# Performance work log

Measured on AMD Instinct MI355X. Metric: run time of the kernel, lower is better.

## Reference

```python
import jax, jax.numpy as jnp
import numpy as np

B, K, VDIM, QDIM, NHID, SE_INNER = 8192, 6, 2048, 1024, 1024, 128

def setup_inputs() -> dict:
    key = jax.random.key(0)
    ks = jax.random.split(key, 10)
    w = lambda k, shape: jax.random.normal(k, shape, dtype=jnp.float32) * 0.02
    return {
        "v": jax.random.normal(ks[0], (B, K, VDIM), dtype=jnp.float32),
        "q": jax.random.normal(ks[1], (B, QDIM), dtype=jnp.float32),
        "mask": (jax.random.uniform(ks[2], (B, K)) > 0.5).astype(jnp.float32),
        "W1": w(ks[3], (NHID, VDIM + QDIM)),   # FCNet weight-normed Linear (effective weight)
        "b1": jnp.zeros((NHID,), jnp.float32),
        "Wl": w(ks[4], (1, NHID)),             # logits Linear(num_hid, 1)
        "bl": jnp.zeros((1,), jnp.float32),
        "Wse1": w(ks[5], (SE_INNER, 1)),       # SELayer fc1, no bias
        "Wse2": w(ks[6], (1, SE_INNER)),       # SELayer fc2, no bias
        "Wf": w(ks[7], (VDIM, 1)),             # final_att_proj Linear(1, v_dim)
        "bf": jnp.zeros((VDIM,), jnp.float32),
    }

def reference(v, q, mask, W1, b1, Wl, bl, Wse1, Wse2, Wf, bf):
    Bn, Kn, _ = v.shape
    # logits(v, q): concat q to every object, FCNet (Linear+ReLU), Linear->1 (dropout is identity at eval)
    qe = jnp.broadcast_to(q[:, None, :], (Bn, Kn, q.shape[-1]))
    vq = jnp.concatenate([v, qe], axis=-1)                       # [B,K,vd+qd]
    joint = jax.nn.relu(jnp.einsum('bkf,hf->bkh', vq, W1) + b1)  # [B,K,NHID]
    logits = jnp.einsum('bkh,oh->bko', joint, Wl) + bl           # [B,K,1]
    single_att = jax.nn.softmax(logits, axis=1)
    w = logits                                                   # view(mask_b, 6, -1) is identity here
    w_ctx = w * mask[..., None]                                  # [B,K,1]
    # per-role sum over the 5 complementary roles == total - self (exact complement index sets)
    neigh = jnp.sum(w_ctx, axis=1, keepdims=True) - w_ctx        # [B,K,1]
    x = neigh[..., None]                                         # [B,K,1,1]
    # SE gate: FC(1->128) -> ReLU -> FC(128->1) -> Sigmoid; out = x * (1 - y)
    y = jax.nn.sigmoid(jax.nn.relu(x @ Wse1.T) @ Wse2.T)          # [B,K,1,1]
    gated = x * (1.0 - y)
    # final_att_proj(gated + w[:,role].unsqueeze(-1)) : Linear(1 -> v_dim)
    upd = (gated + w[..., None]) @ Wf.T + bf                     # [B,K,1,VDIM]
    context_erased_att = upd.reshape(Bn * Kn, 1, upd.shape[-1])  # [B*K,1,VDIM]
    return single_att, context_erased_att
```

## Files before the change

kernel.cpp:

```cpp
#include <hip/hip_runtime.h>

#define B_SZ   8192
#define KOBJ   6
#define VD     2048
#define QD     1024
#define NHID_  1024
#define SEIN   128
#define M_TOT  (B_SZ * KOBJ)
#define K_TOT  (VD + QD)

typedef __bf16 bf16x8 __attribute__((ext_vector_type(8)));
typedef float  f32x4  __attribute__((ext_vector_type(4)));
typedef unsigned int uint4v __attribute__((ext_vector_type(4)));

__device__ __forceinline__ unsigned short f2bf(float f) {
    unsigned u = __builtin_bit_cast(unsigned, f);
    u += 0x7fffu + ((u >> 16) & 1u);
    return (unsigned short)(u >> 16);
}

__global__ __launch_bounds__(256) void conv_w1(const float* __restrict__ W1,
                                               unsigned short* __restrict__ W1b,
                                               int n4) {
    int i = blockIdx.x * 256 + threadIdx.x;
    if (i < n4) {
        float4 f = ((const float4*)W1)[i];
        unsigned lo = (unsigned)f2bf(f.x) | ((unsigned)f2bf(f.y) << 16);
        unsigned hi = (unsigned)f2bf(f.z) | ((unsigned)f2bf(f.w) << 16);
        ((uint2*)W1b)[i] = make_uint2(lo, hi);
    }
}

#define LDA 40
__global__ __launch_bounds__(256) void gemm_logits(
    const float* __restrict__ v, const float* __restrict__ q,
    const unsigned short* __restrict__ W1b,
    const float* __restrict__ b1, const float* __restrict__ Wl,
    float* __restrict__ logits)
{
    __shared__ unsigned short At[128 * LDA];
    __shared__ unsigned short Bt[128 * LDA];

    const int tid  = threadIdx.x;
    const int bid  = blockIdx.x;
    const int nb   = bid & 7;
    const int mb   = bid >> 3;
    const int m0   = mb * 128;
    const int n0   = nb * 128;
    const int wave = tid >> 6, lane = tid & 63;
    const int quad = lane >> 4, l16 = lane & 15;
    const int wr   = (wave >> 1) * 64, wc = (wave & 1) * 64;

    f32x4 acc[4][4] = {};

    for (int kk = 0; kk < K_TOT; kk += 32) {
        __syncthreads();
        const bool isq = (kk >= VD);
        #pragma unroll
        for (int it = 0; it < 4; ++it) {
            int s   = tid + it * 256;
            int row = s >> 3, c4 = s & 7;
            int m   = m0 + row;
            const float* src = isq ? (q + (size_t)(m / KOBJ) * QD + (kk - VD) + c4 * 4)
                                   : (v + (size_t)m * VD + kk + c4 * 4);
            float4 f = *(const float4*)src;
            unsigned lo = (unsigned)f2bf(f.x) | ((unsigned)f2bf(f.y) << 16);
            unsigned hi = (unsigned)f2bf(f.z) | ((unsigned)f2bf(f.w) << 16);
            *(uint2*)&At[row * LDA + c4 * 4] = make_uint2(lo, hi);
        }
        #pragma unroll
        for (int it = 0; it < 2; ++it) {
            int s  = tid + it * 256;
            int n  = s >> 2, kg = s & 3;
            uint4v d = *(const uint4v*)(W1b + (size_t)(n0 + n) * K_TOT + kk + kg * 8);
            *(uint4v*)&Bt[n * LDA + kg * 8] = d;
        }
        __syncthreads();
        bf16x8 af[4], bfr[4];
        #pragma unroll
        for (int i = 0; i < 4; ++i)
            af[i] = __builtin_bit_cast(bf16x8, *(const uint4v*)&At[(wr + i * 16 + l16) * LDA + quad * 8]);
        #pragma unroll
        for (int j = 0; j < 4; ++j)
            bfr[j] = __builtin_bit_cast(bf16x8, *(const uint4v*)&Bt[(wc + j * 16 + l16) * LDA + quad * 8]);
        #pragma unroll
        for (int i = 0; i < 4; ++i)
            #pragma unroll
            for (int j = 0; j < 4; ++j)
                acc[i][j] = __builtin_amdgcn_mfma_f32_16x16x32_bf16(af[i], bfr[j], acc[i][j], 0, 0, 0);
    }

    #pragma unroll
    for (int i = 0; i < 4; ++i) {
        #pragma unroll
        for (int r = 0; r < 4; ++r) {
            int m = m0 + wr + i * 16 + quad * 4 + r;
            float sum = 0.f;
            #pragma unroll
            for (int j = 0; j < 4; ++j) {
                int n = n0 + wc + j * 16 + l16;
                float h = fmaxf(acc[i][j][r] + b1[n], 0.f);
                sum = fmaf(h, Wl[n], sum);
            }
            sum += __shfl_xor(sum, 1);
            sum += __shfl_xor(sum, 2);
            sum += __shfl_xor(sum, 4);
            sum += __shfl_xor(sum, 8);
            if (l16 == 0) atomicAdd(&logits[m], sum);
        }
    }
}

__global__ __launch_bounds__(256) void se_kernel(
    const float* __restrict__ logits, const float* __restrict__ mask,
    const float* __restrict__ bl,
    const float* __restrict__ Wse1, const float* __restrict__ Wse2,
    float* __restrict__ out_att, float* __restrict__ s_buf)
{
    int b = blockIdx.x * 256 + threadIdx.x;
    if (b >= B_SZ) return;
    float w[KOBJ];
    float blv = bl[0];
    #pragma unroll
    for (int k = 0; k < KOBJ; ++k) w[k] = logits[b * KOBJ + k] + blv;

    float mx = w[0];
    #pragma unroll
    for (int k = 1; k < KOBJ; ++k) mx = fmaxf(mx, w[k]);
    float e[KOBJ], den = 0.f;
    #pragma unroll
    for (int k = 0; k < KOBJ; ++k) { e[k] = __expf(w[k] - mx); den += e[k]; }
    float rden = 1.f / den;
    #pragma unroll
    for (int k = 0; k < KOBJ; ++k) out_att[b * KOBJ + k] = e[k] * rden;

    float wc[KOBJ], tot = 0.f;
    #pragma unroll
    for (int k = 0; k < KOBJ; ++k) { wc[k] = w[k] * mask[b * KOBJ + k]; tot += wc[k]; }

    #pragma unroll
    for (int k = 0; k < KOBJ; ++k) {
        float x = tot - wc[k];
        float a = 0.f;
        for (int i = 0; i < SEIN; ++i)
            a = fmaf(fmaxf(x * Wse1[i], 0.f), Wse2[i], a);
        float y = 1.f / (1.f + __expf(-a));
        s_buf[b * KOBJ + k] = x * (1.f - y) + w[k];
    }
}

__global__ __launch_bounds__(256) void out_writer(
    const float* __restrict__ s_buf, const float* __restrict__ Wf,
    const float* __restrict__ bfv, float* __restrict__ out)
{
    int m = blockIdx.x;
    float s = s_buf[m];
    const float4* wf4 = (const float4*)Wf;
    const float4* bf4 = (const float4*)bfv;
    float4* o4 = (float4*)(out + (size_t)m * VD);
    #pragma unroll
    for (int it = 0; it < VD / 4 / 256; ++it) {
        int t = threadIdx.x + it * 256;
        float4 wv = wf4[t], bv = bf4[t];
        float4 r;
        r.x = fmaf(s, wv.x, bv.x);
        r.y = fmaf(s, wv.y, bv.y);
        r.z = fmaf(s, wv.z, bv.z);
        r.w = fmaf(s, wv.w, bv.w);
        o4[t] = r;
    }
}

extern "C" void kernel_launch(void* const* d_in, const int* in_sizes, int n_in,
                              void* d_out, int out_size, void* d_ws, size_t ws_size,
                              hipStream_t stream) {
    const float* v    = (const float*)d_in[0];
    const float* q    = (const float*)d_in[1];
    const float* mask = (const float*)d_in[2];
    const float* W1   = (const float*)d_in[3];
    const float* b1   = (const float*)d_in[4];
    const float* Wl   = (const float*)d_in[5];
    const float* bl   = (const float*)d_in[6];
    const float* Wse1 = (const float*)d_in[7];
    const float* Wse2 = (const float*)d_in[8];
    const float* Wf   = (const float*)d_in[9];
    const float* bfv  = (const float*)d_in[10];
    float* out = (float*)d_out;

    char* ws = (char*)d_ws;
    unsigned short* W1b = (unsigned short*)ws;
    float* logits = (float*)(ws + 6291456);
    float* s_buf  = (float*)(ws + 6291456 + 196608);

    hipMemsetAsync(logits, 0, M_TOT * sizeof(float), stream);
    conv_w1<<<(NHID_ * K_TOT / 4 + 255) / 256, 256, 0, stream>>>(W1, W1b, NHID_ * K_TOT / 4);
    gemm_logits<<<(M_TOT / 128) * (NHID_ / 128), 256, 0, stream>>>(v, q, W1b, b1, Wl, logits);
    se_kernel<<<(B_SZ + 255) / 256, 256, 0, stream>>>(logits, mask, bl, Wse1, Wse2, out, s_buf);
    out_writer<<<M_TOT, 256, 0, stream>>>(s_buf, Wf, bfv, out + M_TOT);
}
```

Baseline: 1.200 ms.

## Pre-convert activations to bf16 and stream GEMM tiles via direct global-to-LDS loads

Adds separate passes that convert v and q to bf16, using the output buffer as scratch, before the GEMM runs. The GEMM then loads bf16 tiles straight into LDS with global_load_lds and reads them with an XOR swizzle instead of padded rows. This is meant to remove per-tile fp32 loads, conversions and register round trips from the GEMM loop, and to halve the bytes each of the eight N-blocks reads for the A operand. In exchange it adds a full extra read and write of v (about 400MB fp32 in, 200MB bf16 out) plus three kernel launches.

```diff
diff --git a/kernel.cpp b/kernel.cpp
--- a/kernel.cpp
+++ b/kernel.cpp
@@ -19,27 +19,30 @@
     return (unsigned short)(u >> 16);
 }
 
-__global__ __launch_bounds__(256) void conv_w1(const float* __restrict__ W1,
-                                               unsigned short* __restrict__ W1b,
-                                               int n4) {
+__global__ __launch_bounds__(256) void conv_bf16(const float* __restrict__ src,
+                                                 unsigned short* __restrict__ dst,
+                                                 int n8) {
     int i = blockIdx.x * 256 + threadIdx.x;
-    if (i < n4) {
-        float4 f = ((const float4*)W1)[i];
-        unsigned lo = (unsigned)f2bf(f.x) | ((unsigned)f2bf(f.y) << 16);
-        unsigned hi = (unsigned)f2bf(f.z) | ((unsigned)f2bf(f.w) << 16);
-        ((uint2*)W1b)[i] = make_uint2(lo, hi);
-    }
-}
-
-#define LDA 40
+    if (i < n8) {
+        float4 f0 = ((const float4*)src)[2 * i];
+        float4 f1 = ((const float4*)src)[2 * i + 1];
+        uint4v d;
+        d[0] = (unsigned)f2bf(f0.x) | ((unsigned)f2bf(f0.y) << 16);
+        d[1] = (unsigned)f2bf(f0.z) | ((unsigned)f2bf(f0.w) << 16);
+        d[2] = (unsigned)f2bf(f1.x) | ((unsigned)f2bf(f1.y) << 16);
+        d[3] = (unsigned)f2bf(f1.z) | ((unsigned)f2bf(f1.w) << 16);
+        ((uint4v*)dst)[i] = d;
+    }
+}
+
 __global__ __launch_bounds__(256) void gemm_logits(
-    const float* __restrict__ v, const float* __restrict__ q,
+    const unsigned short* __restrict__ vb, const unsigned short* __restrict__ qb,
     const unsigned short* __restrict__ W1b,
     const float* __restrict__ b1, const float* __restrict__ Wl,
     float* __restrict__ logits)
 {
-    __shared__ unsigned short At[128 * LDA];
-    __shared__ unsigned short Bt[128 * LDA];
+    __shared__ unsigned short At[128 * 32];
+    __shared__ unsigned short Bt[128 * 32];
 
     const int tid  = threadIdx.x;
     const int bid  = blockIdx.x;
@@ -51,38 +54,56 @@
     const int quad = lane >> 4, l16 = lane & 15;
     const int wr   = (wave >> 1) * 64, wc = (wave & 1) * 64;
 
+    int rowA[2], chA[2];
+    const unsigned short* gav[2];
+    const unsigned short* gaq[2];
+    const unsigned short* gb[2];
+    unsigned short* ldsA[2];
+    unsigned short* ldsB[2];
+    #pragma unroll
+    for (int c = 0; c < 2; ++c) {
+        int seg = wave * 2 + c;
+        rowA[c] = seg * 16 + (lane >> 2);
+        chA[c]  = (lane & 3) ^ ((rowA[c] >> 1) & 3);
+        int m   = m0 + rowA[c];
+        gav[c]  = vb + (size_t)m * VD + chA[c] * 8;
+        gaq[c]  = qb + (size_t)(m / KOBJ) * QD + chA[c] * 8;
+        gb[c]   = W1b + (size_t)(n0 + rowA[c]) * K_TOT + chA[c] * 8;
+        ldsA[c] = &At[seg * 512];
+        ldsB[c] = &Bt[seg * 512];
+    }
+
     f32x4 acc[4][4] = {};
+    const int swz = (l16 >> 1) & 3;
 
     for (int kk = 0; kk < K_TOT; kk += 32) {
         __syncthreads();
         const bool isq = (kk >= VD);
         #pragma unroll
-        for (int it = 0; it < 4; ++it) {
-            int s   = tid + it * 256;
-            int row = s >> 3, c4 = s & 7;
-            int m   = m0 + row;
-            const float* src = isq ? (q + (size_t)(m / KOBJ) * QD + (kk - VD) + c4 * 4)
-                                   : (v + (size_t)m * VD + kk + c4 * 4);
-            float4 f = *(const float4*)src;
-            unsigned lo = (unsigned)f2bf(f.x) | ((unsigned)f2bf(f.y) << 16);
-            unsigned hi = (unsigned)f2bf(f.z) | ((unsigned)f2bf(f.w) << 16);
-            *(uint2*)&At[row * LDA + c4 * 4] = make_uint2(lo, hi);
+        for (int c = 0; c < 2; ++c) {
+            const unsigned short* g = isq ? (gaq[c] + (kk - VD)) : (gav[c] + kk);
+            __builtin_amdgcn_global_load_lds(
+                (const __attribute__((address_space(1))) void*)g,
+                (__attribute__((address_space(3))) void*)ldsA[c], 16, 0, 0);
         }
         #pragma unroll
-        for (int it = 0; it < 2; ++it) {
-            int s  = tid + it * 256;
-            int n  = s >> 2, kg = s & 3;
-            uint4v d = *(const uint4v*)(W1b + (size_t)(n0 + n) * K_TOT + kk + kg * 8);
-            *(uint4v*)&Bt[n * LDA + kg * 8] = d;
+        for (int c = 0; c < 2; ++c) {
+            const unsigned short* g = gb[c] + kk;
+            __builtin_amdgcn_global_load_lds(
+                (const __attribute__((address_space(1))) void*)g,
+                (__attribute__((address_space(3))) void*)ldsB[c], 16, 0, 0);
         }
         __syncthreads();
+
         bf16x8 af[4], bfr[4];
         #pragma unroll
         for (int i = 0; i < 4; ++i)
-            af[i] = __builtin_bit_cast(bf16x8, *(const uint4v*)&At[(wr + i * 16 + l16) * LDA + quad * 8]);
+            af[i] = __builtin_bit_cast(bf16x8,
+                *(const uint4v*)&At[(wr + i * 16 + l16) * 32 + ((quad ^ swz) * 8)]);
         #pragma unroll
         for (int j = 0; j < 4; ++j)
-            bfr[j] = __builtin_bit_cast(bf16x8, *(const uint4v*)&Bt[(wc + j * 16 + l16) * LDA + quad * 8]);
+            bfr[j] = __builtin_bit_cast(bf16x8,
+                *(const uint4v*)&Bt[(wc + j * 16 + l16) * 32 + ((quad ^ swz) * 8)]);
         #pragma unroll
         for (int i = 0; i < 4; ++i)
             #pragma unroll
@@ -134,13 +155,13 @@
     #pragma unroll
     for (int k = 0; k < KOBJ; ++k) out_att[b * KOBJ + k] = e[k] * rden;
 
-    float wc[KOBJ], tot = 0.f;
-    #pragma unroll
-    for (int k = 0; k < KOBJ; ++k) { wc[k] = w[k] * mask[b * KOBJ + k]; tot += wc[k]; }
+    float wcm[KOBJ], tot = 0.f;
+    #pragma unroll
+    for (int k = 0; k < KOBJ; ++k) { wcm[k] = w[k] * mask[b * KOBJ + k]; tot += wcm[k]; }
 
     #pragma unroll
     for (int k = 0; k < KOBJ; ++k) {
-        float x = tot - wc[k];
+        float x = tot - wcm[k];
         float a = 0.f;
         for (int i = 0; i < SEIN; ++i)
             a = fmaf(fmaxf(x * Wse1[i], 0.f), Wse2[i], a);
@@ -192,9 +213,14 @@
     float* logits = (float*)(ws + 6291456);
     float* s_buf  = (float*)(ws + 6291456 + 196608);
 
+    unsigned short* vb = (unsigned short*)((char*)d_out + (size_t)M_TOT * 4);
+    unsigned short* qb = (unsigned short*)((char*)d_out + (size_t)M_TOT * 4 + 201326592);
+
     hipMemsetAsync(logits, 0, M_TOT * sizeof(float), stream);
-    conv_w1<<<(NHID_ * K_TOT / 4 + 255) / 256, 256, 0, stream>>>(W1, W1b, NHID_ * K_TOT / 4);
-    gemm_logits<<<(M_TOT / 128) * (NHID_ / 128), 256, 0, stream>>>(v, q, W1b, b1, Wl, logits);
+    conv_bf16<<<(NHID_ * K_TOT / 8 + 255) / 256, 256, 0, stream>>>(W1, W1b, NHID_ * K_TOT / 8);
+    conv_bf16<<<(M_TOT * VD / 8 + 255) / 256, 256, 0, stream>>>(v, vb, M_TOT * VD / 8);
+    conv_bf16<<<(B_SZ * QD / 8 + 255) / 256, 256, 0, stream>>>(q, qb, B_SZ * QD / 8);
+    gemm_logits<<<(M_TOT / 128) * (NHID_ / 128), 256, 0, stream>>>(vb, qb, W1b, b1, Wl, logits);
     se_kernel<<<(B_SZ + 255) / 256, 256, 0, stream>>>(logits, mask, bl, Wse1, Wse2, out, s_buf);
     out_writer<<<M_TOT, 256, 0, stream>>>(s_buf, Wf, bfv, out + M_TOT);
 }
```

Result: faster. 1.098 ms (-8.5%).
